# Kernel optimization log

Hardware: AMD Instinct MI355X
Metric: run time of the kernel (lower is better)

## Reference

```python
import jax, jax.numpy as jnp
import numpy as np

NEG_INF = -1e30


def setup_inputs() -> dict:
    key = jax.random.key(0)
    ks = jax.random.split(key, 6)
    B, S, D, H, DK = 32, 512, 512, 8, 64
    x = jax.random.normal(ks[0], (B, S, D), dtype=jnp.float32)
    mask = jax.random.randint(ks[1], (B, S), 0, 2, dtype=jnp.int32)
    # xavier-uniform-like scale for [D, DK] projections
    lim_qkv = float(np.sqrt(6.0 / (D + DK)))
    lim_o = float(np.sqrt(6.0 / (D + D)))
    Wq = jax.random.uniform(ks[2], (H, D, DK), jnp.float32, -lim_qkv, lim_qkv)
    Wk = jax.random.uniform(ks[3], (H, D, DK), jnp.float32, -lim_qkv, lim_qkv)
    Wv = jax.random.uniform(ks[4], (H, D, DK), jnp.float32, -lim_qkv, lim_qkv)
    Wo = jax.random.uniform(ks[5], (D, D), jnp.float32, -lim_o, lim_o)
    bias = jnp.zeros((1,), dtype=jnp.float32)
    return {"x": x, "mask": mask, "Wq": Wq, "Wk": Wk, "Wv": Wv, "Wo": Wo, "bias": bias}


def reference(x, mask, Wq, Wk, Wv, Wo, bias):
    B, S, D = x.shape
    H, _, DK = Wq.shape
    scale = 1.0 / jnp.sqrt(jnp.float32(DK))
    # Fused per-head QKV projections (original loops over heads)
    Q = jnp.einsum("bsd,hdk->bhsk", x, Wq) + bias  # [B,H,S,DK]
    K = jnp.einsum("bsd,hdk->bhsk", x, Wk) + bias
    V = jnp.einsum("bsd,hdk->bhsk", x, Wv) + bias
    scores = jnp.einsum("bhsk,bhtk->bhst", Q, K) * scale  # [B,H,S,S]
    # CS224N masked_softmax: mask*logits + (1-mask)*(-1e30), softmax over keys
    m = mask.astype(scores.dtype)[:, None, None, :]  # [B,1,1,S]
    masked = m * scores + (1.0 - m) * NEG_INF
    probs = jax.nn.softmax(masked, axis=-1)
    heads = jnp.einsum("bhst,bhtv->bhsv", probs, V)  # [B,H,S,DK]
    multihead = heads.transpose(0, 2, 1, 3).reshape(B, S, H * DK)  # concat heads
    out = jnp.matmul(multihead, Wo) + bias  # [B,S,D]
    return out
```

## Files before the change

kernel.cpp:

```cpp
#include <hip/hip_runtime.h>
#include <hip/hip_bf16.h>
#include <math.h>

#define NB 32
#define NS 512
#define ND 512
#define NH 8
#define NDK 64

typedef __attribute__((ext_vector_type(8))) short bfrag;
typedef __attribute__((ext_vector_type(4))) float f32x4;

#define SCL 0.18033688011112042592f

__device__ __forceinline__ ushort f2bf(float f) {
    union { float f; unsigned u; } v; v.f = f;
    unsigned u = v.u;
    return (ushort)((u + 0x7fffu + ((u >> 16) & 1u)) >> 16);
}

__device__ __forceinline__ unsigned pk2bf(float a, float b) {
    __hip_bfloat162 h = __float22bfloat162_rn(make_float2(a, b));
    return *reinterpret_cast<unsigned*>(&h);
}

__device__ __forceinline__ void async16(const ushort* g, ushort* l) {
    __builtin_amdgcn_global_load_lds(
        (const __attribute__((address_space(1))) unsigned int*)g,
        (__attribute__((address_space(3))) unsigned int*)l, 16, 0, 0);
}

__global__ __launch_bounds__(256) void cvt_x(const float* __restrict__ x,
                                             ushort* __restrict__ xb) {
    const int idx = blockIdx.x * 256 + threadIdx.x;
    const float4 v = reinterpret_cast<const float4*>(x)[idx];
    ushort4 o;
    o.x = f2bf(v.x); o.y = f2bf(v.y); o.z = f2bf(v.z); o.w = f2bf(v.w);
    reinterpret_cast<ushort4*>(xb)[idx] = o;
}

__global__ __launch_bounds__(256) void cvt_w(const float* __restrict__ Wq,
                                             const float* __restrict__ Wk,
                                             const float* __restrict__ Wv,
                                             const float* __restrict__ Wo,
                                             ushort* __restrict__ WT,
                                             ushort* __restrict__ WoT) {
    __shared__ ushort T[64 * 72];
    const int bid = blockIdx.x, tid = threadIdx.x;
    const float* src; ushort* dst; int d0, n0, stride;
    if (bid < 192) {
        const int which = bid >> 6, h = (bid >> 3) & 7, rt = bid & 7;
        const float* Ws = (which == 0) ? Wq : (which == 1) ? Wk : Wv;
        src = Ws + (size_t)h * ND * NDK;
        dst = WT + (size_t)(which * NH + h) * NDK * ND;
        d0 = rt * 64; n0 = 0; stride = NDK;
    } else {
        const int t = bid - 192, rt = t >> 3, ct = t & 7;
        src = Wo; dst = WoT;
        d0 = rt * 64; n0 = ct * 64; stride = ND;
    }
    #pragma unroll
    for (int i = 0; i < 4; i++) {
        const int u = i * 256 + tid;
        const int row = u >> 4, cq = u & 15;
        const float4 v = *reinterpret_cast<const float4*>(&src[(size_t)(d0 + row) * stride + n0 + cq * 4]);
        T[(cq * 4 + 0) * 72 + row] = f2bf(v.x);
        T[(cq * 4 + 1) * 72 + row] = f2bf(v.y);
        T[(cq * 4 + 2) * 72 + row] = f2bf(v.z);
        T[(cq * 4 + 3) * 72 + row] = f2bf(v.w);
    }
    __syncthreads();
    #pragma unroll
    for (int i = 0; i < 2; i++) {
        const int u = i * 256 + tid;
        const int n = u >> 3, dq = u & 7;
        *reinterpret_cast<float4*>(&dst[(size_t)(n0 + n) * ND + d0 + dq * 8]) =
            *reinterpret_cast<float4*>(&T[n * 72 + dq * 8]);
    }
}

__global__ __launch_bounds__(256) void qkv_mfma(const ushort* __restrict__ xb,
                                                const ushort* __restrict__ WT,
                                                const float* __restrict__ bias,
                                                ushort* __restrict__ Qb,
                                                ushort* __restrict__ Kb,
                                                ushort* __restrict__ VT) {
    __shared__ ushort As[64 * 64];
    __shared__ ushort Bs[64 * 64];
    __shared__ ushort Ts[64 * 72];
    const int id = blockIdx.x;
    const int which = id >> 11;
    const int rem = id & 2047;
    const int b = rem >> 6, h = (rem >> 3) & 7, s0 = (rem & 7) * 64;
    const int tid = threadIdx.x;
    const int wave = tid >> 6, lane = tid & 63, quad = lane >> 4, l16 = lane & 15;
    const int lr = lane >> 3, lc = lane & 7;
    const int cs = lc ^ lr;
    const int swz = l16 & 7;

    const ushort* Wbase = WT + (size_t)(which * NH + h) * NDK * ND;
    const ushort* xbase = xb + ((size_t)b * NS + s0) * ND;

    f32x4 acc[4];
    #pragma unroll
    for (int c = 0; c < 4; c++) acc[c] = (f32x4){0.f, 0.f, 0.f, 0.f};

    for (int d0 = 0; d0 < ND; d0 += 64) {
        __syncthreads();
        #pragma unroll
        for (int t = 0; t < 2; t++) {
            const int rb = (wave * 2 + t) * 8;
            async16(&xbase[(size_t)(rb + lr) * ND + d0 + cs * 8], &As[rb * 64]);
            async16(&Wbase[(size_t)(rb + lr) * ND + d0 + cs * 8], &Bs[rb * 64]);
        }
        __syncthreads();
        #pragma unroll
        for (int ks = 0; ks < 2; ks++) {
            const int ch = ((ks * 4 + quad) ^ swz) * 8;
            const bfrag a = *(const bfrag*)&As[(wave * 16 + l16) * 64 + ch];
            #pragma unroll
            for (int c = 0; c < 4; c++) {
                const bfrag bo = *(const bfrag*)&Bs[(c * 16 + l16) * 64 + ch];
                acc[c] = __builtin_amdgcn_mfma_f32_16x16x32_bf16(a, bo, acc[c], 0, 0, 0);
            }
        }
    }

    const float bb = bias[0];
    if (which < 2) {
        ushort* obase = (which ? Kb : Qb) + ((size_t)(b * NH + h) * NS) * NDK;
        #pragma unroll
        for (int c = 0; c < 4; c++)
            #pragma unroll
            for (int r = 0; r < 4; r++) {
                const int row = s0 + wave * 16 + quad * 4 + r;
                obase[(size_t)row * NDK + c * 16 + l16] = f2bf(acc[c][r] + bb);
            }
    } else {
        #pragma unroll
        for (int c = 0; c < 4; c++)
            #pragma unroll
            for (int r = 0; r < 4; r++)
                Ts[(c * 16 + l16) * 72 + wave * 16 + quad * 4 + r] = f2bf(acc[c][r] + bb);
        __syncthreads();
        ushort* vbase = VT + ((size_t)(b * NH + h) * NDK) * NS;
        const int r0 = tid >> 3, q0 = tid & 7;
        *(float4*)&vbase[(size_t)r0 * NS + s0 + q0 * 8]        = *(float4*)&Ts[r0 * 72 + q0 * 8];
        *(float4*)&vbase[(size_t)(r0 + 32) * NS + s0 + q0 * 8] = *(float4*)&Ts[(r0 + 32) * 72 + q0 * 8];
    }
}

__global__ __launch_bounds__(256) void attn_mfma(const ushort* __restrict__ Qb,
                                                 const ushort* __restrict__ Kb,
                                                 const ushort* __restrict__ VT,
                                                 const int* __restrict__ mask,
                                                 ushort* __restrict__ Hb) {
    __shared__ ushort Qs[64 * 64];
    __shared__ ushort Ks[64 * 64];
    __shared__ ushort Vs[64 * 64];
    __shared__ ushort Ps[64 * 72];
    const int id = blockIdx.x;
    const int b = id >> 6, h = (id >> 3) & 7, s0 = (id & 7) * 64;
    const int tid = threadIdx.x;
    const int wave = tid >> 6, lane = tid & 63, quad = lane >> 4, l16 = lane & 15;
    const int lr = lane >> 3, lc = lane & 7;
    const int cs = lc ^ lr;
    const int swz = l16 & 7;

    const size_t bh = (size_t)(b * NH + h);
    const ushort* qbase = Qb + (bh * NS + s0) * NDK;
    const ushort* kbase = Kb + bh * NS * NDK;
    const ushort* vbase = VT + bh * NDK * NS;

    #pragma unroll
    for (int t = 0; t < 2; t++) {
        const int rb = (wave * 2 + t) * 8;
        async16(&qbase[(size_t)(rb + lr) * NDK + cs * 8], &Qs[rb * 64]);
    }

    float lrow[4] = {0.f, 0.f, 0.f, 0.f};
    f32x4 acc_o[4];
    #pragma unroll
    for (int c = 0; c < 4; c++) acc_o[c] = (f32x4){0.f, 0.f, 0.f, 0.f};

    for (int kt = 0; kt < 8; kt++) {
        __syncthreads();
        const ushort* kb2 = kbase + (size_t)kt * 64 * NDK;
        #pragma unroll
        for (int t = 0; t < 2; t++) {
            const int rb = (wave * 2 + t) * 8;
            const int n = rb + lr;
            const int j = 4 * (n & 15) + (n >> 4);
            async16(&kb2[(size_t)j * NDK + cs * 8], &Ks[rb * 64]);
            async16(&vbase[(size_t)n * NS + kt * 64 + cs * 8], &Vs[rb * 64]);
        }
        __syncthreads();

        f32x4 sc[4];
        #pragma unroll
        for (int c = 0; c < 4; c++) sc[c] = (f32x4){0.f, 0.f, 0.f, 0.f};
        #pragma unroll
        for (int ks = 0; ks < 2; ks++) {
            const int ch = ((ks * 4 + quad) ^ swz) * 8;
            const bfrag a = *(const bfrag*)&Qs[(wave * 16 + l16) * 64 + ch];
            #pragma unroll
            for (int c = 0; c < 4; c++) {
                const bfrag bo = *(const bfrag*)&Ks[(c * 16 + l16) * 64 + ch];
                sc[c] = __builtin_amdgcn_mfma_f32_16x16x32_bf16(a, bo, sc[c], 0, 0, 0);
            }
        }

        const int4 mk4 = *(const int4*)&mask[b * NS + kt * 64 + 4 * l16];
        const int mks[4] = {mk4.x, mk4.y, mk4.z, mk4.w};
        float p[4][4];
        #pragma unroll
        for (int c = 0; c < 4; c++)
            #pragma unroll
            for (int r = 0; r < 4; r++) {
                const float arg = mks[c] ? sc[c][r] * SCL : -INFINITY;
                p[c][r] = exp2f(arg);
            }

        #pragma unroll
        for (int r = 0; r < 4; r++) {
            float rs = (p[0][r] + p[1][r]) + (p[2][r] + p[3][r]);
            rs += __shfl_xor(rs, 1);
            rs += __shfl_xor(rs, 2);
            rs += __shfl_xor(rs, 4);
            rs += __shfl_xor(rs, 8);
            lrow[r] += rs;
            uint2 u;
            u.x = pk2bf(p[0][r], p[1][r]);
            u.y = pk2bf(p[2][r], p[3][r]);
            *(uint2*)&Ps[(wave * 16 + quad * 4 + r) * 72 + l16 * 4] = u;
        }

        #pragma unroll
        for (int ks = 0; ks < 2; ks++) {
            const bfrag a = *(const bfrag*)&Ps[(wave * 16 + l16) * 72 + ks * 32 + quad * 8];
            const int ch = ((ks * 4 + quad) ^ swz) * 8;
            #pragma unroll
            for (int c = 0; c < 4; c++) {
                const bfrag bo = *(const bfrag*)&Vs[(c * 16 + l16) * 64 + ch];
                acc_o[c] = __builtin_amdgcn_mfma_f32_16x16x32_bf16(a, bo, acc_o[c], 0, 0, 0);
            }
        }
    }

    ushort* hbase = Hb + (bh * NS + s0) * NDK;
    #pragma unroll
    for (int r = 0; r < 4; r++) {
        const float inv = 1.0f / lrow[r];
        const int row = wave * 16 + quad * 4 + r;
        #pragma unroll
        for (int c = 0; c < 4; c++)
            hbase[(size_t)row * NDK + c * 16 + l16] = f2bf(acc_o[c][r] * inv);
    }
}

__global__ __launch_bounds__(256) void out_mfma(const ushort* __restrict__ Hb,
                                                const ushort* __restrict__ WoT,
                                                const float* __restrict__ bias,
                                                float* __restrict__ out) {
    __shared__ ushort As[64 * 64];
    __shared__ ushort Bs[64 * 64];
    const int id = blockIdx.x;
    const int b = id >> 6, s0 = ((id >> 3) & 7) * 64, d0 = (id & 7) * 64;
    const int tid = threadIdx.x;
    const int wave = tid >> 6, lane = tid & 63, quad = lane >> 4, l16 = lane & 15;
    const int lr = lane >> 3, lc = lane & 7;
    const int cs = lc ^ lr;
    const int swz = l16 & 15 & 7;

    f32x4 acc[4];
    #pragma unroll
    for (int c = 0; c < 4; c++) acc[c] = (f32x4){0.f, 0.f, 0.f, 0.f};

    for (int h = 0; h < NH; h++) {
        __syncthreads();
        const ushort* hb2 = Hb + (((size_t)b * NH + h) * NS + s0) * NDK;
        const ushort* wb2 = WoT + (size_t)d0 * ND + h * 64;
        #pragma unroll
        for (int t = 0; t < 2; t++) {
            const int rb = (wave * 2 + t) * 8;
            async16(&hb2[(size_t)(rb + lr) * NDK + cs * 8], &As[rb * 64]);
            async16(&wb2[(size_t)(rb + lr) * ND + cs * 8], &Bs[rb * 64]);
        }
        __syncthreads();
        #pragma unroll
        for (int ks = 0; ks < 2; ks++) {
            const int ch = ((ks * 4 + quad) ^ swz) * 8;
            const bfrag a = *(const bfrag*)&As[(wave * 16 + l16) * 64 + ch];
            #pragma unroll
            for (int c = 0; c < 4; c++) {
                const bfrag bo = *(const bfrag*)&Bs[(c * 16 + l16) * 64 + ch];
                acc[c] = __builtin_amdgcn_mfma_f32_16x16x32_bf16(a, bo, acc[c], 0, 0, 0);
            }
        }
    }

    const float bb = bias[0];
    float* obase = out + ((size_t)b * NS + s0) * ND + d0;
    #pragma unroll
    for (int c = 0; c < 4; c++)
        #pragma unroll
        for (int r = 0; r < 4; r++)
            obase[(size_t)(wave * 16 + quad * 4 + r) * ND + c * 16 + l16] = acc[c][r] + bb;
}

extern "C" void kernel_launch(void* const* d_in, const int* in_sizes, int n_in,
                              void* d_out, int out_size, void* d_ws, size_t ws_size,
                              hipStream_t stream) {
    const float* x    = (const float*)d_in[0];
    const int*   mask = (const int*)  d_in[1];
    const float* Wq   = (const float*)d_in[2];
    const float* Wk   = (const float*)d_in[3];
    const float* Wv   = (const float*)d_in[4];
    const float* Wo   = (const float*)d_in[5];
    const float* bias = (const float*)d_in[6];
    float* out = (float*)d_out;

    const size_t TE = (size_t)NB * NH * NS * NDK;
    ushort* xb  = (ushort*)d_ws;
    ushort* WT  = xb  + TE;
    ushort* WoT = WT  + (size_t)3 * NH * NDK * ND;
    ushort* Qb  = WoT + (size_t)ND * ND;
    ushort* Kb  = Qb  + TE;
    ushort* VT  = Kb  + TE;
    ushort* Hb  = VT  + TE;

    cvt_x<<<dim3((NB * NS * ND) / 1024), dim3(256), 0, stream>>>(x, xb);
    cvt_w<<<dim3(256), dim3(256), 0, stream>>>(Wq, Wk, Wv, Wo, WT, WoT);
    qkv_mfma<<<dim3(3 * NB * NH * (NS / 64)), dim3(256), 0, stream>>>(
        xb, WT, bias, Qb, Kb, VT);
    attn_mfma<<<dim3(NB * NH * (NS / 64)), dim3(256), 0, stream>>>(
        Qb, Kb, VT, mask, Hb);
    out_mfma<<<dim3(NB * (NS / 64) * (ND / 64)), dim3(256), 0, stream>>>(
        Hb, WoT, bias, out);
}
```

Measured before the change: 211.5 us.

## Use 128x128 GEMM tiles for QK/out projections, separate V^T GEMM, MFMA row sums

Replaces the 64x64-tile per-head QKV projection with a 128x128-tile GEMM for Q and K that writes a row-major interleaved [B*S, 1024] buffer. V^T gets its own GEMM computed as W_v^T x^T, so the transpose no longer goes through shared memory. The output projection moves to 128x128 tiles over a row-major head buffer, and attention computes softmax row sums with an MFMA against a ones vector instead of cross-lane shuffles. The larger tiles are meant to improve data reuse and MFMA density. In exchange they use more registers and LDS per block, and the Q/K rows are strided, which costs some locality in the attention kernel.

```diff
diff --git a/kernel.cpp b/kernel.cpp
--- a/kernel.cpp
+++ b/kernel.cpp
@@ -79,79 +79,134 @@
     }
 }
 
-__global__ __launch_bounds__(256) void qkv_mfma(const ushort* __restrict__ xb,
-                                                const ushort* __restrict__ WT,
-                                                const float* __restrict__ bias,
-                                                ushort* __restrict__ Qb,
-                                                ushort* __restrict__ Kb,
-                                                ushort* __restrict__ VT) {
+__global__ __launch_bounds__(256) void qk_gemm(const ushort* __restrict__ xb,
+                                               const ushort* __restrict__ WT,
+                                               const float* __restrict__ bias,
+                                               ushort* __restrict__ QKb) {
+    __shared__ ushort As[128 * 64];
+    __shared__ ushort Bs[128 * 64];
+    const int bid = blockIdx.x;
+    const int m0 = (bid & 127) * 128, n0 = (bid >> 7) * 128;
+    const int tid = threadIdx.x;
+    const int w = tid >> 6, lane = tid & 63, quad = lane >> 4, l16 = lane & 15;
+    const int lr = lane >> 3, lc = lane & 7, cs = lc ^ lr, swz = l16 & 7;
+    const int rw = (w & 1) * 64, cw = (w >> 1) * 64;
+
+    f32x4 acc[4][4];
+    #pragma unroll
+    for (int i = 0; i < 4; i++)
+        #pragma unroll
+        for (int j = 0; j < 4; j++) acc[i][j] = (f32x4){0.f, 0.f, 0.f, 0.f};
+
+    for (int d0 = 0; d0 < ND; d0 += 64) {
+        __syncthreads();
+        #pragma unroll
+        for (int t = 0; t < 4; t++) {
+            const int rb = (w * 4 + t) * 8;
+            async16(&xb[(size_t)(m0 + rb + lr) * ND + d0 + cs * 8], &As[rb * 64]);
+            const int slot = rb + lr, nn = slot & 63;
+            const int j = n0 + (slot & 64) + 4 * (nn & 15) + (nn >> 4);
+            async16(&WT[(size_t)j * ND + d0 + cs * 8], &Bs[rb * 64]);
+        }
+        __syncthreads();
+        #pragma unroll
+        for (int ks = 0; ks < 2; ks++) {
+            const int ch = ((ks * 4 + quad) ^ swz) * 8;
+            bfrag a[4], bo[4];
+            #pragma unroll
+            for (int rf = 0; rf < 4; rf++) a[rf] = *(const bfrag*)&As[(rw + rf * 16 + l16) * 64 + ch];
+            #pragma unroll
+            for (int cf = 0; cf < 4; cf++) bo[cf] = *(const bfrag*)&Bs[(cw + cf * 16 + l16) * 64 + ch];
+            #pragma unroll
+            for (int rf = 0; rf < 4; rf++)
+                #pragma unroll
+                for (int cf = 0; cf < 4; cf++)
+                    acc[rf][cf] = __builtin_amdgcn_mfma_f32_16x16x32_bf16(a[rf], bo[cf], acc[rf][cf], 0, 0, 0);
+        }
+    }
+
+    const float bb = bias[0];
+    #pragma unroll
+    for (int rf = 0; rf < 4; rf++)
+        #pragma unroll
+        for (int r = 0; r < 4; r++) {
+            const int row = m0 + rw + rf * 16 + quad * 4 + r;
+            uint2 u;
+            u.x = pk2bf(acc[rf][0][r] + bb, acc[rf][1][r] + bb);
+            u.y = pk2bf(acc[rf][2][r] + bb, acc[rf][3][r] + bb);
+            *(uint2*)&QKb[(size_t)row * 1024 + n0 + cw + 4 * l16] = u;
+        }
+}
+
+__global__ __launch_bounds__(256) void vt_gemm(const ushort* __restrict__ xb,
+                                               const ushort* __restrict__ WT,
+                                               const float* __restrict__ bias,
+                                               ushort* __restrict__ VT) {
     __shared__ ushort As[64 * 64];
-    __shared__ ushort Bs[64 * 64];
-    __shared__ ushort Ts[64 * 72];
-    const int id = blockIdx.x;
-    const int which = id >> 11;
-    const int rem = id & 2047;
-    const int b = rem >> 6, h = (rem >> 3) & 7, s0 = (rem & 7) * 64;
+    __shared__ ushort Bs[256 * 64];
+    const int bid = blockIdx.x;
+    const int bh = bid >> 1, s0 = (bid & 1) * 256;
+    const int b = bh >> 3, h = bh & 7;
     const int tid = threadIdx.x;
-    const int wave = tid >> 6, lane = tid & 63, quad = lane >> 4, l16 = lane & 15;
-    const int lr = lane >> 3, lc = lane & 7;
-    const int cs = lc ^ lr;
-    const int swz = l16 & 7;
-
-    const ushort* Wbase = WT + (size_t)(which * NH + h) * NDK * ND;
-    const ushort* xbase = xb + ((size_t)b * NS + s0) * ND;
-
-    f32x4 acc[4];
-    #pragma unroll
-    for (int c = 0; c < 4; c++) acc[c] = (f32x4){0.f, 0.f, 0.f, 0.f};
+    const int w = tid >> 6, lane = tid & 63, quad = lane >> 4, l16 = lane & 15;
+    const int lr = lane >> 3, lc = lane & 7, cs = lc ^ lr, swz = l16 & 7;
+    const int cw = w * 64;
+
+    const ushort* Av = WT + (size_t)(2 * NH + h) * NDK * ND;
+    const ushort* xrow = xb + (size_t)b * NS * ND;
+
+    f32x4 acc[4][4];
+    #pragma unroll
+    for (int i = 0; i < 4; i++)
+        #pragma unroll
+        for (int j = 0; j < 4; j++) acc[i][j] = (f32x4){0.f, 0.f, 0.f, 0.f};
 
     for (int d0 = 0; d0 < ND; d0 += 64) {
         __syncthreads();
         #pragma unroll
         for (int t = 0; t < 2; t++) {
-            const int rb = (wave * 2 + t) * 8;
-            async16(&xbase[(size_t)(rb + lr) * ND + d0 + cs * 8], &As[rb * 64]);
-            async16(&Wbase[(size_t)(rb + lr) * ND + d0 + cs * 8], &Bs[rb * 64]);
-        }
-        __syncthreads();
-        #pragma unroll
-        for (int ks = 0; ks < 2; ks++) {
-            const int ch = ((ks * 4 + quad) ^ swz) * 8;
-            const bfrag a = *(const bfrag*)&As[(wave * 16 + l16) * 64 + ch];
-            #pragma unroll
-            for (int c = 0; c < 4; c++) {
-                const bfrag bo = *(const bfrag*)&Bs[(c * 16 + l16) * 64 + ch];
-                acc[c] = __builtin_amdgcn_mfma_f32_16x16x32_bf16(a, bo, acc[c], 0, 0, 0);
-            }
+            const int rb = w * 16 + t * 8;
+            async16(&Av[(size_t)(rb + lr) * ND + d0 + cs * 8], &As[rb * 64]);
+        }
+        #pragma unroll
+        for (int t = 0; t < 8; t++) {
+            const int rb = (w * 8 + t) * 8;
+            const int slot = rb + lr, nn = slot & 63;
+            const int js = s0 + (slot & 192) + 4 * (nn & 15) + (nn >> 4);
+            async16(&xrow[(size_t)js * ND + d0 + cs * 8], &Bs[rb * 64]);
+        }
+        __syncthreads();
+        #pragma unroll
+        for (int ks = 0; ks < 2; ks++) {
+            const int ch = ((ks * 4 + quad) ^ swz) * 8;
+            bfrag a[4], bo[4];
+            #pragma unroll
+            for (int rf = 0; rf < 4; rf++) a[rf] = *(const bfrag*)&As[(rf * 16 + l16) * 64 + ch];
+            #pragma unroll
+            for (int cf = 0; cf < 4; cf++) bo[cf] = *(const bfrag*)&Bs[(cw + cf * 16 + l16) * 64 + ch];
+            #pragma unroll
+            for (int rf = 0; rf < 4; rf++)
+                #pragma unroll
+                for (int cf = 0; cf < 4; cf++)
+                    acc[rf][cf] = __builtin_amdgcn_mfma_f32_16x16x32_bf16(a[rf], bo[cf], acc[rf][cf], 0, 0, 0);
         }
     }
 
     const float bb = bias[0];
-    if (which < 2) {
-        ushort* obase = (which ? Kb : Qb) + ((size_t)(b * NH + h) * NS) * NDK;
-        #pragma unroll
-        for (int c = 0; c < 4; c++)
-            #pragma unroll
-            for (int r = 0; r < 4; r++) {
-                const int row = s0 + wave * 16 + quad * 4 + r;
-                obase[(size_t)row * NDK + c * 16 + l16] = f2bf(acc[c][r] + bb);
-            }
-    } else {
-        #pragma unroll
-        for (int c = 0; c < 4; c++)
-            #pragma unroll
-            for (int r = 0; r < 4; r++)
-                Ts[(c * 16 + l16) * 72 + wave * 16 + quad * 4 + r] = f2bf(acc[c][r] + bb);
-        __syncthreads();
-        ushort* vbase = VT + ((size_t)(b * NH + h) * NDK) * NS;
-        const int r0 = tid >> 3, q0 = tid & 7;
-        *(float4*)&vbase[(size_t)r0 * NS + s0 + q0 * 8]        = *(float4*)&Ts[r0 * 72 + q0 * 8];
-        *(float4*)&vbase[(size_t)(r0 + 32) * NS + s0 + q0 * 8] = *(float4*)&Ts[(r0 + 32) * 72 + q0 * 8];
-    }
-}
-
-__global__ __launch_bounds__(256) void attn_mfma(const ushort* __restrict__ Qb,
-                                                 const ushort* __restrict__ Kb,
+    ushort* vbase = VT + (size_t)bh * NDK * NS;
+    #pragma unroll
+    for (int rf = 0; rf < 4; rf++)
+        #pragma unroll
+        for (int r = 0; r < 4; r++) {
+            const int dk = rf * 16 + quad * 4 + r;
+            uint2 u;
+            u.x = pk2bf(acc[rf][0][r] + bb, acc[rf][1][r] + bb);
+            u.y = pk2bf(acc[rf][2][r] + bb, acc[rf][3][r] + bb);
+            *(uint2*)&vbase[(size_t)dk * NS + s0 + cw + 4 * l16] = u;
+        }
+}
+
+__global__ __launch_bounds__(256) void attn_mfma(const ushort* __restrict__ QKb,
                                                  const ushort* __restrict__ VT,
                                                  const int* __restrict__ mask,
                                                  ushort* __restrict__ Hb) {
@@ -163,36 +218,36 @@
     const int b = id >> 6, h = (id >> 3) & 7, s0 = (id & 7) * 64;
     const int tid = threadIdx.x;
     const int wave = tid >> 6, lane = tid & 63, quad = lane >> 4, l16 = lane & 15;
-    const int lr = lane >> 3, lc = lane & 7;
-    const int cs = lc ^ lr;
-    const int swz = l16 & 7;
-
-    const size_t bh = (size_t)(b * NH + h);
-    const ushort* qbase = Qb + (bh * NS + s0) * NDK;
-    const ushort* kbase = Kb + bh * NS * NDK;
-    const ushort* vbase = VT + bh * NDK * NS;
+    const int lr = lane >> 3, lc = lane & 7, cs = lc ^ lr, swz = l16 & 7;
+
+    const ushort* qbase = QKb + (size_t)(b * NS + s0) * 1024 + h * 64;
+    const ushort* kbase = QKb + (size_t)(b * NS) * 1024 + 512 + h * 64;
+    const ushort* vbase = VT + (size_t)(b * NH + h) * NDK * NS;
 
     #pragma unroll
     for (int t = 0; t < 2; t++) {
         const int rb = (wave * 2 + t) * 8;
-        async16(&qbase[(size_t)(rb + lr) * NDK + cs * 8], &Qs[rb * 64]);
-    }
-
-    float lrow[4] = {0.f, 0.f, 0.f, 0.f};
+        async16(&qbase[(size_t)(rb + lr) * 1024 + cs * 8], &Qs[rb * 64]);
+    }
+
+    bfrag ones;
+    #pragma unroll
+    for (int i = 0; i < 8; i++) ones[i] = (short)0x3F80;
+
+    f32x4 acc_l = (f32x4){0.f, 0.f, 0.f, 0.f};
     f32x4 acc_o[4];
     #pragma unroll
     for (int c = 0; c < 4; c++) acc_o[c] = (f32x4){0.f, 0.f, 0.f, 0.f};
 
     for (int kt = 0; kt < 8; kt++) {
         __syncthreads();
-        const ushort* kb2 = kbase + (size_t)kt * 64 * NDK;
         #pragma unroll
         for (int t = 0; t < 2; t++) {
             const int rb = (wave * 2 + t) * 8;
             const int n = rb + lr;
-            const int j = 4 * (n & 15) + (n >> 4);
-            async16(&kb2[(size_t)j * NDK + cs * 8], &Ks[rb * 64]);
-            async16(&vbase[(size_t)n * NS + kt * 64 + cs * 8], &Vs[rb * 64]);
+            const int jk = 4 * (n & 15) + (n >> 4);
+            async16(&kbase[(size_t)(kt * 64 + jk) * 1024 + cs * 8], &Ks[rb * 64]);
+            async16(&vbase[(size_t)jk * NS + kt * 64 + cs * 8], &Vs[rb * 64]);
         }
         __syncthreads();
 
@@ -212,32 +267,26 @@
 
         const int4 mk4 = *(const int4*)&mask[b * NS + kt * 64 + 4 * l16];
         const int mks[4] = {mk4.x, mk4.y, mk4.z, mk4.w};
-        float p[4][4];
-        #pragma unroll
-        for (int c = 0; c < 4; c++)
-            #pragma unroll
-            for (int r = 0; r < 4; r++) {
-                const float arg = mks[c] ? sc[c][r] * SCL : -INFINITY;
-                p[c][r] = exp2f(arg);
-            }
-
+        #pragma unroll
+        for (int c = 0; c < 4; c++) {
+            float p[4];
+            #pragma unroll
+            for (int r = 0; r < 4; r++)
+                p[r] = exp2f(mks[c] ? sc[c][r] * SCL : -INFINITY);
+            sc[c][0] = p[0]; sc[c][1] = p[1]; sc[c][2] = p[2]; sc[c][3] = p[3];
+        }
         #pragma unroll
         for (int r = 0; r < 4; r++) {
-            float rs = (p[0][r] + p[1][r]) + (p[2][r] + p[3][r]);
-            rs += __shfl_xor(rs, 1);
-            rs += __shfl_xor(rs, 2);
-            rs += __shfl_xor(rs, 4);
-            rs += __shfl_xor(rs, 8);
-            lrow[r] += rs;
             uint2 u;
-            u.x = pk2bf(p[0][r], p[1][r]);
-            u.y = pk2bf(p[2][r], p[3][r]);
+            u.x = pk2bf(sc[0][r], sc[1][r]);
+            u.y = pk2bf(sc[2][r], sc[3][r]);
             *(uint2*)&Ps[(wave * 16 + quad * 4 + r) * 72 + l16 * 4] = u;
         }
 
         #pragma unroll
         for (int ks = 0; ks < 2; ks++) {
             const bfrag a = *(const bfrag*)&Ps[(wave * 16 + l16) * 72 + ks * 32 + quad * 8];
+            acc_l = __builtin_amdgcn_mfma_f32_16x16x32_bf16(a, ones, acc_l, 0, 0, 0);
             const int ch = ((ks * 4 + quad) ^ swz) * 8;
             #pragma unroll
             for (int c = 0; c < 4; c++) {
@@ -247,65 +296,75 @@
         }
     }
 
-    ushort* hbase = Hb + (bh * NS + s0) * NDK;
+    ushort* hbase = Hb + (size_t)(b * NS + s0) * ND + h * 64;
     #pragma unroll
     for (int r = 0; r < 4; r++) {
-        const float inv = 1.0f / lrow[r];
+        const float inv = 1.0f / acc_l[r];
         const int row = wave * 16 + quad * 4 + r;
-        #pragma unroll
-        for (int c = 0; c < 4; c++)
-            hbase[(size_t)row * NDK + c * 16 + l16] = f2bf(acc_o[c][r] * inv);
-    }
-}
-
-__global__ __launch_bounds__(256) void out_mfma(const ushort* __restrict__ Hb,
+        uint2 u;
+        u.x = pk2bf(acc_o[0][r] * inv, acc_o[1][r] * inv);
+        u.y = pk2bf(acc_o[2][r] * inv, acc_o[3][r] * inv);
+        *(uint2*)&hbase[(size_t)row * ND + 4 * l16] = u;
+    }
+}
+
+__global__ __launch_bounds__(256) void out_gemm(const ushort* __restrict__ Hb,
                                                 const ushort* __restrict__ WoT,
                                                 const float* __restrict__ bias,
                                                 float* __restrict__ out) {
-    __shared__ ushort As[64 * 64];
-    __shared__ ushort Bs[64 * 64];
-    const int id = blockIdx.x;
-    const int b = id >> 6, s0 = ((id >> 3) & 7) * 64, d0 = (id & 7) * 64;
+    __shared__ ushort As[128 * 64];
+    __shared__ ushort Bs[128 * 64];
+    const int bid = blockIdx.x;
+    const int m0 = (bid & 127) * 128, n0 = (bid >> 7) * 128;
     const int tid = threadIdx.x;
-    const int wave = tid >> 6, lane = tid & 63, quad = lane >> 4, l16 = lane & 15;
-    const int lr = lane >> 3, lc = lane & 7;
-    const int cs = lc ^ lr;
-    const int swz = l16 & 15 & 7;
-
-    f32x4 acc[4];
-    #pragma unroll
-    for (int c = 0; c < 4; c++) acc[c] = (f32x4){0.f, 0.f, 0.f, 0.f};
-
-    for (int h = 0; h < NH; h++) {
-        __syncthreads();
-        const ushort* hb2 = Hb + (((size_t)b * NH + h) * NS + s0) * NDK;
-        const ushort* wb2 = WoT + (size_t)d0 * ND + h * 64;
-        #pragma unroll
-        for (int t = 0; t < 2; t++) {
-            const int rb = (wave * 2 + t) * 8;
-            async16(&hb2[(size_t)(rb + lr) * NDK + cs * 8], &As[rb * 64]);
-            async16(&wb2[(size_t)(rb + lr) * ND + cs * 8], &Bs[rb * 64]);
-        }
-        __syncthreads();
-        #pragma unroll
-        for (int ks = 0; ks < 2; ks++) {
-            const int ch = ((ks * 4 + quad) ^ swz) * 8;
-            const bfrag a = *(const bfrag*)&As[(wave * 16 + l16) * 64 + ch];
-            #pragma unroll
-            for (int c = 0; c < 4; c++) {
-                const bfrag bo = *(const bfrag*)&Bs[(c * 16 + l16) * 64 + ch];
-                acc[c] = __builtin_amdgcn_mfma_f32_16x16x32_bf16(a, bo, acc[c], 0, 0, 0);
-            }
+    const int w = tid >> 6, lane = tid & 63, quad = lane >> 4, l16 = lane & 15;
+    const int lr = lane >> 3, lc = lane & 7, cs = lc ^ lr, swz = l16 & 7;
+    const int rw = (w & 1) * 64, cw = (w >> 1) * 64;
+
+    f32x4 acc[4][4];
+    #pragma unroll
+    for (int i = 0; i < 4; i++)
+        #pragma unroll
+        for (int j = 0; j < 4; j++) acc[i][j] = (f32x4){0.f, 0.f, 0.f, 0.f};
+
+    for (int d0 = 0; d0 < ND; d0 += 64) {
+        __syncthreads();
+        #pragma unroll
+        for (int t = 0; t < 4; t++) {
+            const int rb = (w * 4 + t) * 8;
+            async16(&Hb[(size_t)(m0 + rb + lr) * ND + d0 + cs * 8], &As[rb * 64]);
+            const int slot = rb + lr, nn = slot & 63;
+            const int j = n0 + (slot & 64) + 4 * (nn & 15) + (nn >> 4);
+            async16(&WoT[(size_t)j * ND + d0 + cs * 8], &Bs[rb * 64]);
+        }
+        __syncthreads();
+        #pragma unroll
+        for (int ks = 0; ks < 2; ks++) {
+            const int ch = ((ks * 4 + quad) ^ swz) * 8;
+            bfrag a[4], bo[4];
+            #pragma unroll
+            for (int rf = 0; rf < 4; rf++) a[rf] = *(const bfrag*)&As[(rw + rf * 16 + l16) * 64 + ch];
+            #pragma unroll
+            for (int cf = 0; cf < 4; cf++) bo[cf] = *(const bfrag*)&Bs[(cw + cf * 16 + l16) * 64 + ch];
+            #pragma unroll
+            for (int rf = 0; rf < 4; rf++)
+                #pragma unroll
+                for (int cf = 0; cf < 4; cf++)
+                    acc[rf][cf] = __builtin_amdgcn_mfma_f32_16x16x32_bf16(a[rf], bo[cf], acc[rf][cf], 0, 0, 0);
         }
     }
 
     const float bb = bias[0];
-    float* obase = out + ((size_t)b * NS + s0) * ND + d0;
-    #pragma unroll
-    for (int c = 0; c < 4; c++)
-        #pragma unroll
-        for (int r = 0; r < 4; r++)
-            obase[(size_t)(wave * 16 + quad * 4 + r) * ND + c * 16 + l16] = acc[c][r] + bb;
+    #pragma unroll
+    for (int rf = 0; rf < 4; rf++)
+        #pragma unroll
+        for (int r = 0; r < 4; r++) {
+            const int row = m0 + rw + rf * 16 + quad * 4 + r;
+            float4 v;
+            v.x = acc[rf][0][r] + bb; v.y = acc[rf][1][r] + bb;
+            v.z = acc[rf][2][r] + bb; v.w = acc[rf][3][r] + bb;
+            *(float4*)&out[(size_t)row * ND + n0 + cw + 4 * l16] = v;
+        }
 }
 
 extern "C" void kernel_launch(void* const* d_in, const int* in_sizes, int n_in,
@@ -320,21 +379,19 @@
     const float* bias = (const float*)d_in[6];
     float* out = (float*)d_out;
 
-    const size_t TE = (size_t)NB * NH * NS * NDK;
+    const size_t TE = (size_t)NB * NS * ND;
     ushort* xb  = (ushort*)d_ws;
     ushort* WT  = xb  + TE;
     ushort* WoT = WT  + (size_t)3 * NH * NDK * ND;
-    ushort* Qb  = WoT + (size_t)ND * ND;
-    ushort* Kb  = Qb  + TE;
-    ushort* VT  = Kb  + TE;
+    ushort* QKb = WoT + (size_t)ND * ND;
+    ushort* VT  = QKb + (size_t)NB * NS * 2 * ND;
     ushort* Hb  = VT  + TE;
 
     cvt_x<<<dim3((NB * NS * ND) / 1024), dim3(256), 0, stream>>>(x, xb);
     cvt_w<<<dim3(256), dim3(256), 0, stream>>>(Wq, Wk, Wv, Wo, WT, WoT);
-    qkv_mfma<<<dim3(3 * NB * NH * (NS / 64)), dim3(256), 0, stream>>>(
-        xb, WT, bias, Qb, Kb, VT);
+    qk_gemm<<<dim3(1024), dim3(256), 0, stream>>>(xb, WT, bias, QKb);
+    vt_gemm<<<dim3(512), dim3(256), 0, stream>>>(xb, WT, bias, VT);
     attn_mfma<<<dim3(NB * NH * (NS / 64)), dim3(256), 0, stream>>>(
-        Qb, Kb, VT, mask, Hb);
-    out_mfma<<<dim3(NB * (NS / 64) * (ND / 64)), dim3(256), 0, stream>>>(
-        Hb, WoT, bias, out);
-}
+        QKb, VT, mask, Hb);
+    out_gemm<<<dim3(512), dim3(256), 0, stream>>>(Hb, WoT, bias, out);
+}
```

New measurement: 198.5 us. -6.2%, faster.
